# Kernel tuning notes

Hardware: AMD Instinct MI355X
Metric: run time of the kernel (lower is better)

## Reference

```python
import jax, jax.numpy as jnp
import numpy as np

B, T, C = 2, 4096, 512
H, DH = 8, 64            # num_heads, num_head_channels (per-head dim after reshape)
COND = 512
SCALE = (DH // H) ** -0.5  # faithful to original: (num_head_channels // num_heads)**-0.5


def setup_inputs() -> dict:
    key = jax.random.key(0)
    ks = jax.random.split(key, 6)
    x = jax.random.normal(ks[0], (B, T, C), dtype=jnp.float32)
    condition = jax.random.normal(ks[1], (B, T, COND), dtype=jnp.float32)
    W_qk = jax.random.normal(ks[2], (COND, 2 * H * DH), dtype=jnp.float32) * (COND ** -0.5)
    W_v = jax.random.normal(ks[3], (C, H * DH), dtype=jnp.float32) * (C ** -0.5)
    W_u = jax.random.normal(ks[4], (H * DH, C), dtype=jnp.float32) * ((H * DH) ** -0.5)
    b_u = jax.random.normal(ks[5], (C,), dtype=jnp.float32) * 0.01
    return {"x": x, "condition": condition, "W_qk": W_qk, "W_v": W_v, "W_u": W_u, "b_u": b_u}


def reference(x, condition, W_qk, W_v, W_u, b_u):
    b, t, _ = x.shape
    qk = condition @ W_qk                                  # [b, t, 2*H*DH]
    q, k = jnp.split(qk, 2, axis=-1)
    q = q.reshape(b, t, H, DH).transpose(0, 2, 1, 3)       # [b, H, t, DH]
    k = k.reshape(b, t, H, DH).transpose(0, 2, 1, 3)
    v = (x @ W_v).reshape(b, t, H, DH).transpose(0, 2, 1, 3)
    q = q * SCALE
    dots = jnp.einsum('bhid,bhjd->bhij', q, k)             # [b, H, t, t] (1 GB score matrix)
    attn = jax.nn.softmax(dots, axis=-1)
    out = jnp.einsum('bhij,bhjd->bhid', attn, v)           # [b, H, t, DH]
    out = out.transpose(0, 2, 1, 3).reshape(b, t, H * DH)
    return out @ W_u + b_u
```

## Files before the change

kernel.cpp:

```cpp
#include <hip/hip_runtime.h>

#define B_SZ 2
#define T_SZ 4096

typedef unsigned short u16;
typedef __attribute__((ext_vector_type(8))) short short8;
typedef __attribute__((ext_vector_type(4))) float f32x4;
typedef __attribute__((ext_vector_type(4))) unsigned short u16x4;

#define CEXP 0.51006973f

__device__ __forceinline__ u16 f2bf(float f) {
    unsigned int u;
    __builtin_memcpy(&u, &f, 4);
    u = (u + 0x7fffu + ((u >> 16) & 1u)) >> 16;
    return (u16)u;
}
__device__ __forceinline__ unsigned int rbits(float f) {
    unsigned int u;
    __builtin_memcpy(&u, &f, 4);
    return u + 0x8000u;
}
__device__ __forceinline__ f32x4 mfma16(short8 a, short8 b, f32x4 c) {
    return __builtin_amdgcn_mfma_f32_16x16x32_bf16(a, b, c, 0, 0, 0);
}

__global__ void k_prep(const float* __restrict__ x, const float* __restrict__ cond,
                       const float* __restrict__ Wqk, const float* __restrict__ Wv,
                       const float* __restrict__ Wu, u16* __restrict__ xb, u16* __restrict__ cb,
                       u16* __restrict__ Wqk_t, u16* __restrict__ Wv_t, u16* __restrict__ Wu_t) {
    int blk = blockIdx.x;
    if (blk < 8192) {
        const float* s = blk < 4096 ? x : cond;
        u16* d = blk < 4096 ? xb : cb;
        int i = ((blk & 4095) * 256 + threadIdx.x) * 4;
        float4 v = *(const float4*)(s + i);
        u16x4 o = { f2bf(v.x), f2bf(v.y), f2bf(v.z), f2bf(v.w) };
        *(u16x4*)(d + i) = o;
    } else if (blk < 10240) {
        int idx = (blk - 8192) * 256 + threadIdx.x;
        Wqk_t[(size_t)(idx & 1023) * 512 + (idx >> 10)] = f2bf(Wqk[idx]);
    } else if (blk < 11264) {
        int idx = (blk - 10240) * 256 + threadIdx.x;
        Wv_t[(size_t)(idx & 511) * 512 + (idx >> 9)] = f2bf(Wv[idx]);
    } else {
        int idx = (blk - 11264) * 256 + threadIdx.x;
        Wu_t[(size_t)(idx & 511) * 512 + (idx >> 9)] = f2bf(Wu[idx]);
    }
}

template <typename OutT, int MODE, int TM, int TN>
__global__ __launch_bounds__(256) void k_gemm3(const u16* __restrict__ A, const u16* __restrict__ Bt,
                                               const float* __restrict__ bias, OutT* __restrict__ C,
                                               OutT* __restrict__ C2) {
    const int K = 512;
    constexpr int MI = TM / 32, NJ = TN / 32;
    constexpr int NA = TM / 64, NB = TN / 64;
    int m0 = blockIdx.x * TM, n0 = blockIdx.y * TN;
    int tid = threadIdx.x;
    int wave = tid >> 6, lane = tid & 63, l16 = lane & 15, q = lane >> 4;
    int mo = (wave & 1) * (TM / 2), no = (wave >> 1) * (TN / 2);

    __shared__ __align__(16) u16 As[TM * 72];
    __shared__ __align__(16) u16 Bs[TN * 72];

    f32x4 acc[MI][NJ];
#pragma unroll
    for (int i = 0; i < MI; ++i)
#pragma unroll
        for (int j = 0; j < NJ; ++j) acc[i][j] = (f32x4){0.f, 0.f, 0.f, 0.f};

    const u16* ap[NA]; const u16* bp[NB];
    short8 ra[NA], rb[NB];
#pragma unroll
    for (int jj = 0; jj < NA; ++jj) {
        int id = tid + 256 * jj;
        ap[jj] = A + (size_t)(m0 + (id >> 2)) * K + (id & 3) * 8;
        ra[jj] = *(const short8*)(ap[jj]);
    }
#pragma unroll
    for (int jj = 0; jj < NB; ++jj) {
        int id = tid + 256 * jj;
        bp[jj] = Bt + (size_t)(n0 + (id >> 2)) * K + (id & 3) * 8;
        rb[jj] = *(const short8*)(bp[jj]);
    }

#pragma unroll 1
    for (int k0 = 0; k0 < K; k0 += 32) {
        __syncthreads();
#pragma unroll
        for (int jj = 0; jj < NA; ++jj) {
            int id = tid + 256 * jj;
            *(short8*)(&As[(id >> 2) * 72 + (id & 3) * 8]) = ra[jj];
        }
#pragma unroll
        for (int jj = 0; jj < NB; ++jj) {
            int id = tid + 256 * jj;
            *(short8*)(&Bs[(id >> 2) * 72 + (id & 3) * 8]) = rb[jj];
        }
        __syncthreads();

        int kadv = (k0 + 32 < K) ? 32 : 0;
#pragma unroll
        for (int jj = 0; jj < NA; ++jj) { ap[jj] += kadv; ra[jj] = *(const short8*)(ap[jj]); }
#pragma unroll
        for (int jj = 0; jj < NB; ++jj) { bp[jj] += kadv; rb[jj] = *(const short8*)(bp[jj]); }
        __builtin_amdgcn_sched_barrier(0);

        short8 af[MI], bf[NJ];
#pragma unroll
        for (int i = 0; i < MI; ++i) af[i] = *(const short8*)(&As[(mo + i * 16 + l16) * 72 + q * 8]);
#pragma unroll
        for (int j = 0; j < NJ; ++j) bf[j] = *(const short8*)(&Bs[(no + j * 16 + l16) * 72 + q * 8]);
#pragma unroll
        for (int i = 0; i < MI; ++i)
#pragma unroll
            for (int j = 0; j < NJ; ++j) acc[i][j] = mfma16(af[i], bf[j], acc[i][j]);
    }

#pragma unroll
    for (int i = 0; i < MI; ++i) {
        int chb = m0 + mo + i * 16 + q * 4;
#pragma unroll
        for (int j = 0; j < NJ; ++j) {
            int trow = n0 + no + j * 16 + l16;
            if constexpr (MODE == 0) {
                float4 bb = *(const float4*)(bias + chb);
                float4 w = { acc[i][j][0] + bb.x, acc[i][j][1] + bb.y,
                             acc[i][j][2] + bb.z, acc[i][j][3] + bb.w };
                *(float4*)(&C[(size_t)trow * 512 + chb]) = w;
            } else if constexpr (MODE == 1) {
                int b = trow >> 12, t = trow & 4095;
                int h = (chb & 511) >> 6, d = chb & 63;
                size_t addr = ((size_t)((b * 8 + h) * 4096 + t)) * 64 + d;
                if (chb < 512) {
                    u16x4 w = { f2bf(acc[i][j][0] * CEXP), f2bf(acc[i][j][1] * CEXP),
                                f2bf(acc[i][j][2] * CEXP), f2bf(acc[i][j][3] * CEXP) };
                    *(u16x4*)(&C[addr]) = w;
                } else {
                    u16x4 w = { f2bf(acc[i][j][0]), f2bf(acc[i][j][1]),
                                f2bf(acc[i][j][2]), f2bf(acc[i][j][3]) };
                    *(u16x4*)(&C2[addr]) = w;
                }
            } else {
                int b = trow >> 12, t = trow & 4095;
                int kt = t >> 6, k64 = t & 63;
                int h = chb >> 6;
#pragma unroll
                for (int r = 0; r < 4; ++r) {
                    int d = (chb + r) & 63;
                    size_t addr = ((((size_t)(b * 8 + h) * 64 + kt) * 64 + d) << 6) + k64;
                    C[addr] = f2bf(acc[i][j][r]);
                }
            }
        }
    }
}

__global__ __launch_bounds__(256) void k_flash(const u16* __restrict__ Qh, const u16* __restrict__ Kh,
                                               const u16* __restrict__ Vb, u16* __restrict__ o) {
    int qt = blockIdx.x, h = blockIdx.y, b = blockIdx.z;
    int tid = threadIdx.x;
    int wave = tid >> 6, lane = tid & 63, l16 = lane & 15, q = lane >> 4;

    __shared__ __align__(16) u16 Kt[64 * 80];
    __shared__ __align__(16) u16 Vt[64 * 72];

    int head = b * 8 + h;
    const u16* qp = Qh + ((size_t)head * 4096 + qt * 64 + wave * 16 + l16) * 64 + q * 8;
    short8 qf0 = *(const short8*)(qp);
    short8 qf1 = *(const short8*)(qp + 32);

    const u16* kc = Kh + (size_t)head * 4096 * 64;
    const u16* vc = Vb + (size_t)head * 4096 * 64;

    int r0 = tid >> 3, g0 = tid & 7;
    u16* kw0 = &Kt[r0 * 80 + g0 * 8];
    u16* kw1 = &Kt[(r0 + 32) * 80 + g0 * 8];
    u16* vw0 = &Vt[r0 * 72 + g0 * 8];
    u16* vw1 = &Vt[(r0 + 32) * 72 + g0 * 8];

    f32x4 oacc[4];
#pragma unroll
    for (int c = 0; c < 4; ++c) oacc[c] = (f32x4){0.f, 0.f, 0.f, 0.f};
    f32x4 lacc = (f32x4){0.f, 0.f, 0.f, 0.f};
    const short8 ones = { 0x3F80, 0x3F80, 0x3F80, 0x3F80, 0x3F80, 0x3F80, 0x3F80, 0x3F80 };
    int pi0 = (l16 >> 2) * 8 + (l16 & 3);

    short8 rk0 = *(const short8*)(kc + tid * 8);
    short8 rk1 = *(const short8*)(kc + tid * 8 + 2048);
    short8 rv0 = *(const short8*)(vc + tid * 8);
    short8 rv1 = *(const short8*)(vc + tid * 8 + 2048);

#pragma unroll 1
    for (int kt = 0; kt < 64; ++kt) {
        __syncthreads();
        *(short8*)kw0 = rk0;
        *(short8*)kw1 = rk1;
        *(short8*)vw0 = rv0;
        *(short8*)vw1 = rv1;
        __syncthreads();

        int adv = (kt < 63) ? 4096 : 0;
        kc += adv; vc += adv;
        rk0 = *(const short8*)(kc + tid * 8);
        rk1 = *(const short8*)(kc + tid * 8 + 2048);
        rv0 = *(const short8*)(vc + tid * 8);
        rv1 = *(const short8*)(vc + tid * 8 + 2048);
        __builtin_amdgcn_sched_barrier(0);

#pragma unroll
        for (int kk = 0; kk < 2; ++kk) {
            const u16* ka = &Kt[(kk * 32 + pi0) * 80 + q * 8];
            short8 A00 = *(const short8*)(ka);
            short8 A01 = *(const short8*)(ka + 32);
            short8 A10 = *(const short8*)(ka + 4 * 80);
            short8 A11 = *(const short8*)(ka + 4 * 80 + 32);
            f32x4 s0 = (f32x4){0.f, 0.f, 0.f, 0.f};
            f32x4 s1 = (f32x4){0.f, 0.f, 0.f, 0.f};
            s0 = mfma16(A00, qf0, s0); s0 = mfma16(A01, qf1, s0);
            s1 = mfma16(A10, qf0, s1); s1 = mfma16(A11, qf1, s1);

            uint4 pd;
            pd.x = __builtin_amdgcn_perm(rbits(__builtin_amdgcn_exp2f(s0[1])),
                                         rbits(__builtin_amdgcn_exp2f(s0[0])), 0x07060302u);
            pd.y = __builtin_amdgcn_perm(rbits(__builtin_amdgcn_exp2f(s0[3])),
                                         rbits(__builtin_amdgcn_exp2f(s0[2])), 0x07060302u);
            pd.z = __builtin_amdgcn_perm(rbits(__builtin_amdgcn_exp2f(s1[1])),
                                         rbits(__builtin_amdgcn_exp2f(s1[0])), 0x07060302u);
            pd.w = __builtin_amdgcn_perm(rbits(__builtin_amdgcn_exp2f(s1[3])),
                                         rbits(__builtin_amdgcn_exp2f(s1[2])), 0x07060302u);
            short8 pf;
            __builtin_memcpy(&pf, &pd, 16);

            lacc = mfma16(ones, pf, lacc);
#pragma unroll
            for (int c = 0; c < 4; ++c) {
                short8 vfc = *(const short8*)(&Vt[(c * 16 + l16) * 72 + kk * 32 + q * 8]);
                oacc[c] = mfma16(vfc, pf, oacc[c]);
            }
        }
    }

    float inv = 1.f / lacc[0];

    u16* ob = o + (size_t)(b * T_SZ + qt * 64 + wave * 16 + l16) * 512 + h * 64 + q * 4;
#pragma unroll
    for (int c = 0; c < 4; ++c) {
        u16x4 w = { f2bf(oacc[c][0] * inv), f2bf(oacc[c][1] * inv),
                    f2bf(oacc[c][2] * inv), f2bf(oacc[c][3] * inv) };
        *(u16x4*)(ob + c * 16) = w;
    }
}

extern "C" void kernel_launch(void* const* d_in, const int* in_sizes, int n_in,
                              void* d_out, int out_size, void* d_ws, size_t ws_size,
                              hipStream_t stream) {
    const float* x    = (const float*)d_in[0];
    const float* cond = (const float*)d_in[1];
    const float* Wqk  = (const float*)d_in[2];
    const float* Wv   = (const float*)d_in[3];
    const float* Wu   = (const float*)d_in[4];
    const float* bu   = (const float*)d_in[5];
    float* out = (float*)d_out;

    const size_t MT = (size_t)B_SZ * T_SZ;
    u16* xb    = (u16*)d_ws;
    u16* cb    = xb + MT * 512;
    u16* qh_ws = cb + MT * 512;
    u16* kh_ws = qh_ws + MT * 512;
    u16* vb_ws = kh_ws + MT * 512;
    u16* at_ws = vb_ws + MT * 512;
    u16* Wqk_t = at_ws + MT * 512;
    u16* Wv_t  = Wqk_t + (size_t)1024 * 512;
    u16* Wu_t  = Wv_t + (size_t)512 * 512;

    k_prep<<<12288, 256, 0, stream>>>(x, cond, Wqk, Wv, Wu, xb, cb, Wqk_t, Wv_t, Wu_t);

    k_gemm3<u16, 1, 256, 64><<<dim3(4, 128), 256, 0, stream>>>(Wqk_t, cb, nullptr, qh_ws, kh_ws);
    k_gemm3<u16, 2, 128, 64><<<dim3(4, 128), 256, 0, stream>>>(Wv_t, xb, nullptr, vb_ws, nullptr);
    k_flash<<<dim3(64, 8, 2), 256, 0, stream>>>(qh_ws, kh_ws, vb_ws, at_ws);
    k_gemm3<float, 0, 128, 64><<<dim3(4, 128), 256, 0, stream>>>(Wu_t, at_ws, bu, out, nullptr);
}
```

Measured before the change: 238.5 us.

## Split flash KV range across wave groups, reshape GEMM tiles and V-store layout

After: 221.9 us. -7.0%, faster.

```diff
diff --git a/kernel.cpp b/kernel.cpp
--- a/kernel.cpp
+++ b/kernel.cpp
@@ -50,7 +50,7 @@
 }
 
 template <typename OutT, int MODE, int TM, int TN>
-__global__ __launch_bounds__(256) void k_gemm3(const u16* __restrict__ A, const u16* __restrict__ Bt,
+__global__ __launch_bounds__(256) void k_gemm5(const u16* __restrict__ A, const u16* __restrict__ Bt,
                                                const float* __restrict__ bias, OutT* __restrict__ C,
                                                OutT* __restrict__ C2) {
     const int K = 512;
@@ -120,20 +120,20 @@
 
 #pragma unroll
     for (int i = 0; i < MI; ++i) {
-        int chb = m0 + mo + i * 16 + q * 4;
+        int mb = m0 + mo + i * 16 + q * 4;
 #pragma unroll
         for (int j = 0; j < NJ; ++j) {
-            int trow = n0 + no + j * 16 + l16;
+            int nc = n0 + no + j * 16 + l16;
             if constexpr (MODE == 0) {
-                float4 bb = *(const float4*)(bias + chb);
+                float4 bb = *(const float4*)(bias + mb);
                 float4 w = { acc[i][j][0] + bb.x, acc[i][j][1] + bb.y,
                              acc[i][j][2] + bb.z, acc[i][j][3] + bb.w };
-                *(float4*)(&C[(size_t)trow * 512 + chb]) = w;
+                *(float4*)(&C[(size_t)nc * 512 + mb]) = w;
             } else if constexpr (MODE == 1) {
-                int b = trow >> 12, t = trow & 4095;
-                int h = (chb & 511) >> 6, d = chb & 63;
+                int b = nc >> 12, t = nc & 4095;
+                int h = (mb & 511) >> 6, d = mb & 63;
                 size_t addr = ((size_t)((b * 8 + h) * 4096 + t)) * 64 + d;
-                if (chb < 512) {
+                if (mb < 512) {
                     u16x4 w = { f2bf(acc[i][j][0] * CEXP), f2bf(acc[i][j][1] * CEXP),
                                 f2bf(acc[i][j][2] * CEXP), f2bf(acc[i][j][3] * CEXP) };
                     *(u16x4*)(&C[addr]) = w;
@@ -143,57 +143,68 @@
                     *(u16x4*)(&C2[addr]) = w;
                 }
             } else {
-                int b = trow >> 12, t = trow & 4095;
+                int b = mb >> 12, t = mb & 4095;
                 int kt = t >> 6, k64 = t & 63;
-                int h = chb >> 6;
-#pragma unroll
-                for (int r = 0; r < 4; ++r) {
-                    int d = (chb + r) & 63;
-                    size_t addr = ((((size_t)(b * 8 + h) * 64 + kt) * 64 + d) << 6) + k64;
-                    C[addr] = f2bf(acc[i][j][r]);
-                }
+                int h = nc >> 6, d = nc & 63;
+                size_t addr = ((((size_t)(b * 8 + h) * 64 + kt) * 64 + d) << 6) + k64;
+                u16x4 w = { f2bf(acc[i][j][0]), f2bf(acc[i][j][1]),
+                            f2bf(acc[i][j][2]), f2bf(acc[i][j][3]) };
+                *(u16x4*)(&C[addr]) = w;
             }
         }
     }
 }
 
-__global__ __launch_bounds__(256) void k_flash(const u16* __restrict__ Qh, const u16* __restrict__ Kh,
+__global__ __launch_bounds__(512) void k_flash(const u16* __restrict__ Qh, const u16* __restrict__ Kh,
                                                const u16* __restrict__ Vb, u16* __restrict__ o) {
-    int qt = blockIdx.x, h = blockIdx.y, b = blockIdx.z;
+    int bid = blockIdx.x;
+    int h = bid & 7, qt = (bid >> 3) & 31, b = bid >> 8;
     int tid = threadIdx.x;
     int wave = tid >> 6, lane = tid & 63, l16 = lane & 15, q = lane >> 4;
-
-    __shared__ __align__(16) u16 Kt[64 * 80];
-    __shared__ __align__(16) u16 Vt[64 * 72];
+    int ks = wave >> 2, w4 = wave & 3;
+    int t256 = tid & 255;
+
+    __shared__ __align__(16) u16 smem[2 * (64 * 80 + 64 * 72)];
+    u16* Kt = smem + ks * (64 * 80 + 64 * 72);
+    u16* Vt = Kt + 64 * 80;
 
     int head = b * 8 + h;
-    const u16* qp = Qh + ((size_t)head * 4096 + qt * 64 + wave * 16 + l16) * 64 + q * 8;
-    short8 qf0 = *(const short8*)(qp);
-    short8 qf1 = *(const short8*)(qp + 32);
-
-    const u16* kc = Kh + (size_t)head * 4096 * 64;
-    const u16* vc = Vb + (size_t)head * 4096 * 64;
-
-    int r0 = tid >> 3, g0 = tid & 7;
+    short8 qf[2][2];
+#pragma unroll
+    for (int g = 0; g < 2; ++g) {
+        const u16* qp = Qh + ((size_t)head * 4096 + qt * 128 + g * 64 + w4 * 16 + l16) * 64 + q * 8;
+        qf[g][0] = *(const short8*)(qp);
+        qf[g][1] = *(const short8*)(qp + 32);
+    }
+
+    const u16* kb = Kh + (size_t)head * 4096 * 64;
+    const u16* vb = Vb + (size_t)head * 4096 * 64;
+
+    int r0 = t256 >> 3, g0 = t256 & 7;
     u16* kw0 = &Kt[r0 * 80 + g0 * 8];
     u16* kw1 = &Kt[(r0 + 32) * 80 + g0 * 8];
     u16* vw0 = &Vt[r0 * 72 + g0 * 8];
     u16* vw1 = &Vt[(r0 + 32) * 72 + g0 * 8];
 
-    f32x4 oacc[4];
-#pragma unroll
-    for (int c = 0; c < 4; ++c) oacc[c] = (f32x4){0.f, 0.f, 0.f, 0.f};
-    f32x4 lacc = (f32x4){0.f, 0.f, 0.f, 0.f};
+    f32x4 oacc[2][4];
+#pragma unroll
+    for (int g = 0; g < 2; ++g)
+#pragma unroll
+        for (int c = 0; c < 4; ++c) oacc[g][c] = (f32x4){0.f, 0.f, 0.f, 0.f};
+    f32x4 lacc[2];
+    lacc[0] = (f32x4){0.f, 0.f, 0.f, 0.f};
+    lacc[1] = (f32x4){0.f, 0.f, 0.f, 0.f};
     const short8 ones = { 0x3F80, 0x3F80, 0x3F80, 0x3F80, 0x3F80, 0x3F80, 0x3F80, 0x3F80 };
     int pi0 = (l16 >> 2) * 8 + (l16 & 3);
 
-    short8 rk0 = *(const short8*)(kc + tid * 8);
-    short8 rk1 = *(const short8*)(kc + tid * 8 + 2048);
-    short8 rv0 = *(const short8*)(vc + tid * 8);
-    short8 rv1 = *(const short8*)(vc + tid * 8 + 2048);
+    size_t off0 = (size_t)(ks * 32 + (qt & 31)) * 4096;
+    short8 rk0 = *(const short8*)(kb + off0 + t256 * 8);
+    short8 rk1 = *(const short8*)(kb + off0 + t256 * 8 + 2048);
+    short8 rv0 = *(const short8*)(vb + off0 + t256 * 8);
+    short8 rv1 = *(const short8*)(vb + off0 + t256 * 8 + 2048);
 
 #pragma unroll 1
-    for (int kt = 0; kt < 64; ++kt) {
+    for (int it = 0; it < 32; ++it) {
         __syncthreads();
         *(short8*)kw0 = rk0;
         *(short8*)kw1 = rk1;
@@ -201,12 +212,11 @@
         *(short8*)vw1 = rv1;
         __syncthreads();
 
-        int adv = (kt < 63) ? 4096 : 0;
-        kc += adv; vc += adv;
-        rk0 = *(const short8*)(kc + tid * 8);
-        rk1 = *(const short8*)(kc + tid * 8 + 2048);
-        rv0 = *(const short8*)(vc + tid * 8);
-        rv1 = *(const short8*)(vc + tid * 8 + 2048);
+        size_t offn = (size_t)(ks * 32 + ((qt + it + 1) & 31)) * 4096;
+        rk0 = *(const short8*)(kb + offn + t256 * 8);
+        rk1 = *(const short8*)(kb + offn + t256 * 8 + 2048);
+        rv0 = *(const short8*)(vb + offn + t256 * 8);
+        rv1 = *(const short8*)(vb + offn + t256 * 8 + 2048);
         __builtin_amdgcn_sched_barrier(0);
 
 #pragma unroll
@@ -216,40 +226,69 @@
             short8 A01 = *(const short8*)(ka + 32);
             short8 A10 = *(const short8*)(ka + 4 * 80);
             short8 A11 = *(const short8*)(ka + 4 * 80 + 32);
-            f32x4 s0 = (f32x4){0.f, 0.f, 0.f, 0.f};
-            f32x4 s1 = (f32x4){0.f, 0.f, 0.f, 0.f};
-            s0 = mfma16(A00, qf0, s0); s0 = mfma16(A01, qf1, s0);
-            s1 = mfma16(A10, qf0, s1); s1 = mfma16(A11, qf1, s1);
-
-            uint4 pd;
-            pd.x = __builtin_amdgcn_perm(rbits(__builtin_amdgcn_exp2f(s0[1])),
-                                         rbits(__builtin_amdgcn_exp2f(s0[0])), 0x07060302u);
-            pd.y = __builtin_amdgcn_perm(rbits(__builtin_amdgcn_exp2f(s0[3])),
-                                         rbits(__builtin_amdgcn_exp2f(s0[2])), 0x07060302u);
-            pd.z = __builtin_amdgcn_perm(rbits(__builtin_amdgcn_exp2f(s1[1])),
-                                         rbits(__builtin_amdgcn_exp2f(s1[0])), 0x07060302u);
-            pd.w = __builtin_amdgcn_perm(rbits(__builtin_amdgcn_exp2f(s1[3])),
-                                         rbits(__builtin_amdgcn_exp2f(s1[2])), 0x07060302u);
-            short8 pf;
-            __builtin_memcpy(&pf, &pd, 16);
-
-            lacc = mfma16(ones, pf, lacc);
+            short8 vfc[4];
+#pragma unroll
+            for (int c = 0; c < 4; ++c)
+                vfc[c] = *(const short8*)(&Vt[(c * 16 + l16) * 72 + kk * 32 + q * 8]);
+
+#pragma unroll
+            for (int g = 0; g < 2; ++g) {
+                f32x4 s0 = (f32x4){0.f, 0.f, 0.f, 0.f};
+                f32x4 s1 = (f32x4){0.f, 0.f, 0.f, 0.f};
+                s0 = mfma16(A00, qf[g][0], s0); s0 = mfma16(A01, qf[g][1], s0);
+                s1 = mfma16(A10, qf[g][0], s1); s1 = mfma16(A11, qf[g][1], s1);
+
+                uint4 pd;
+                pd.x = __builtin_amdgcn_perm(rbits(__builtin_amdgcn_exp2f(s0[1])),
+                                             rbits(__builtin_amdgcn_exp2f(s0[0])), 0x07060302u);
+                pd.y = __builtin_amdgcn_perm(rbits(__builtin_amdgcn_exp2f(s0[3])),
+                                             rbits(__builtin_amdgcn_exp2f(s0[2])), 0x07060302u);
+                pd.z = __builtin_amdgcn_perm(rbits(__builtin_amdgcn_exp2f(s1[1])),
+                                             rbits(__builtin_amdgcn_exp2f(s1[0])), 0x07060302u);
+                pd.w = __builtin_amdgcn_perm(rbits(__builtin_amdgcn_exp2f(s1[3])),
+                                             rbits(__builtin_amdgcn_exp2f(s1[2])), 0x07060302u);
+                short8 pf;
+                __builtin_memcpy(&pf, &pd, 16);
+
+                lacc[g] = mfma16(ones, pf, lacc[g]);
+#pragma unroll
+                for (int c = 0; c < 4; ++c)
+                    oacc[g][c] = mfma16(vfc[c], pf, oacc[g][c]);
+            }
+        }
+    }
+
+    __syncthreads();
+    float* red = (float*)smem;
+    if (ks == 1) {
+        float* rp = red + ((w4 * 64 + lane) * 37);
+#pragma unroll
+        for (int g = 0; g < 2; ++g)
+#pragma unroll
+            for (int c = 0; c < 4; ++c)
+#pragma unroll
+                for (int r = 0; r < 4; ++r) rp[g * 16 + c * 4 + r] = oacc[g][c][r];
+        rp[32] = lacc[0][0];
+        rp[33] = lacc[1][0];
+    }
+    __syncthreads();
+    if (ks == 0) {
+        const float* rp = red + ((w4 * 64 + lane) * 37);
+#pragma unroll
+        for (int g = 0; g < 2; ++g) {
+#pragma unroll
+            for (int c = 0; c < 4; ++c)
+#pragma unroll
+                for (int r = 0; r < 4; ++r) oacc[g][c][r] += rp[g * 16 + c * 4 + r];
+            float inv = 1.f / (lacc[g][0] + rp[32 + g]);
+            u16* ob = o + (size_t)(b * T_SZ + qt * 128 + g * 64 + w4 * 16 + l16) * 512 + h * 64 + q * 4;
 #pragma unroll
             for (int c = 0; c < 4; ++c) {
-                short8 vfc = *(const short8*)(&Vt[(c * 16 + l16) * 72 + kk * 32 + q * 8]);
-                oacc[c] = mfma16(vfc, pf, oacc[c]);
+                u16x4 w = { f2bf(oacc[g][c][0] * inv), f2bf(oacc[g][c][1] * inv),
+                            f2bf(oacc[g][c][2] * inv), f2bf(oacc[g][c][3] * inv) };
+                *(u16x4*)(ob + c * 16) = w;
             }
         }
-    }
-
-    float inv = 1.f / lacc[0];
-
-    u16* ob = o + (size_t)(b * T_SZ + qt * 64 + wave * 16 + l16) * 512 + h * 64 + q * 4;
-#pragma unroll
-    for (int c = 0; c < 4; ++c) {
-        u16x4 w = { f2bf(oacc[c][0] * inv), f2bf(oacc[c][1] * inv),
-                    f2bf(oacc[c][2] * inv), f2bf(oacc[c][3] * inv) };
-        *(u16x4*)(ob + c * 16) = w;
     }
 }
 
@@ -277,8 +316,8 @@
 
     k_prep<<<12288, 256, 0, stream>>>(x, cond, Wqk, Wv, Wu, xb, cb, Wqk_t, Wv_t, Wu_t);
 
-    k_gemm3<u16, 1, 256, 64><<<dim3(4, 128), 256, 0, stream>>>(Wqk_t, cb, nullptr, qh_ws, kh_ws);
-    k_gemm3<u16, 2, 128, 64><<<dim3(4, 128), 256, 0, stream>>>(Wv_t, xb, nullptr, vb_ws, nullptr);
-    k_flash<<<dim3(64, 8, 2), 256, 0, stream>>>(qh_ws, kh_ws, vb_ws, at_ws);
-    k_gemm3<float, 0, 128, 64><<<dim3(4, 128), 256, 0, stream>>>(Wu_t, at_ws, bu, out, nullptr);
-}
+    k_gemm5<u16, 1, 128, 64><<<dim3(8, 128), 256, 0, stream>>>(Wqk_t, cb, nullptr, qh_ws, kh_ws);
+    k_gemm5<u16, 2, 64, 64><<<dim3(128, 8), 256, 0, stream>>>(xb, Wv_t, nullptr, vb_ws, nullptr);
+    k_flash<<<512, 512, 0, stream>>>(qh_ws, kh_ws, vb_ws, at_ws);
+    k_gemm5<float, 0, 64, 64><<<dim3(8, 128), 256, 0, stream>>>(Wu_t, at_ws, bu, out, nullptr);
+}
```
